# Optimization experiments

Hardware: AMD Instinct MI355X
Metric: run time of the kernel (lower is better)

The kernel has to match this reference:

```python
import jax, jax.numpy as jnp
import numpy as np

LOG2PI = float(np.log(2.0 * np.pi))
CLIP_LO, CLIP_HI = 1e-6, 1.0 - 1e-6


def gaussian_log_prob(X, mu):
    # X: (s, d), mu: (K, d) -> (s, K); unit-variance diagonal Normal.
    d = X.shape[-1]
    sq = (
        (X * X).sum(-1, keepdims=True)
        - 2.0 * (X @ mu.T)
        + (mu * mu).sum(-1)[None, :]
    )
    return -0.5 * (sq + d * LOG2PI)


def setup_inputs() -> dict:
    key = jax.random.key(0)
    kz, ks, kd, km1, km2 = jax.random.split(key, 5)
    s, K, n, dz = 60000, 200, 6, 64
    Z = jax.random.normal(kz, (s, dz), dtype=jnp.float32)
    S = jax.random.normal(ks, (s, 3), dtype=jnp.float32)
    D = jax.random.randint(kd, (s, n), 0, s, dtype=jnp.int64)
    sel_mu = jax.random.normal(km1, (K, dz), dtype=jnp.float32)
    spa_mu = jax.random.normal(km2, (K, 3), dtype=jnp.float32)
    return {"Z": Z, "S": S, "D": D, "sel_mu": sel_mu, "spa_mu": spa_mu}


def reference(Z, S, D, sel_mu, spa_mu):
    # point energy U: (s, K)
    U = -(gaussian_log_prob(Z, sel_mu) + gaussian_log_prob(S, spa_mu))
    Q = jax.nn.softmax(-U, axis=-1)  # temperature = 1.0
    # expected point energy: (s,)
    point = (Q * U).sum(-1)
    # doublet energy: gather neighbor rows, coassignment, potential, mask
    Qc = jnp.clip(Q, CLIP_LO, CLIP_HI)
    co = jnp.einsum('snk,sk->sn', Qc[D], Qc)  # (s, n)
    doublet = jnp.where(D < 0, 0.0, -jnp.log(co)).sum(-1)  # (s,)
    return point + doublet
```

## Files before the change

kernel.cpp:

```cpp
#include <hip/hip_runtime.h>
#include <math.h>

#define KK 200
#define NT 13
#define NNB 6

typedef __attribute__((ext_vector_type(8))) short short8;
typedef __attribute__((ext_vector_type(4))) float f32x4;
#define MFMA16 __builtin_amdgcn_mfma_f32_16x16x32_bf16

__device__ __forceinline__ unsigned short bfh(float f) {
    unsigned u = __float_as_uint(f);
    return (unsigned short)((u + 0x7fffu + ((u >> 16) & 1u)) >> 16);
}
__device__ __forceinline__ float bf2f(unsigned short h) {
    return __uint_as_float(((unsigned)h) << 16);
}
__device__ __forceinline__ short8 z8() {
    short8 v;
#pragma unroll
    for (int j = 0; j < 8; ++j) v[j] = 0;
    return v;
}
__device__ __forceinline__ void cv2(float f, short8& hi, short8& lo, int j) {
    unsigned short h = bfh(f);
    hi[j] = (short)h;
    lo[j] = (short)bfh(f - bf2f(h));
}

__global__ __launch_bounds__(512, 4) void
k_point(const float* __restrict__ Z, const float* __restrict__ S,
        const float* __restrict__ selmu, const float* __restrict__ spamu,
        unsigned short* __restrict__ Qc, float* __restrict__ pointbuf,
        int sRows, int mTiles)
{
    __shared__ short8 ldsBh[26 * 64];
    __shared__ short8 ldsBl[26 * 64];
    __shared__ uint2  ldsB2h[NT * 16];
    __shared__ uint2  ldsB2l[NT * 16];

    const int tid = threadIdx.x;

    for (int slot = tid; slot < 26 * 64; slot += 512) {
        int L = slot & 63, ts = slot >> 6;
        int t = ts >> 1, sstep = ts & 1;
        int n = t * 16 + (L & 15);
        int kb = sstep * 32 + (L >> 4) * 8;
        short8 hi = z8(), lo = z8();
        if (n < KK) {
            const float* mp = selmu + (size_t)n * 64 + kb;
            float4 a = *(const float4*)mp;
            float4 b = *(const float4*)(mp + 4);
            cv2(a.x, hi, lo, 0); cv2(a.y, hi, lo, 1); cv2(a.z, hi, lo, 2); cv2(a.w, hi, lo, 3);
            cv2(b.x, hi, lo, 4); cv2(b.y, hi, lo, 5); cv2(b.z, hi, lo, 6); cv2(b.w, hi, lo, 7);
        }
        ldsBh[slot] = hi;
        ldsBl[slot] = lo;
    }
    if (tid < NT * 16) {
        int n = tid;
        uint2 vh = make_uint2(0, 0), vl = make_uint2(0, 0);
        if (n < KK) {
            float p0 = spamu[n * 3 + 0], p1 = spamu[n * 3 + 1], p2 = spamu[n * 3 + 2];
            float nrm = p0 * p0 + p1 * p1 + p2 * p2;
            const float* mp = selmu + (size_t)n * 64;
#pragma unroll 8
            for (int k = 0; k < 64; ++k) { float m = mp[k]; nrm = fmaf(m, m, nrm); }
            nrm *= -0.5f;
            unsigned short h0 = bfh(p0), h1 = bfh(p1), h2 = bfh(p2), h3 = bfh(nrm);
            unsigned short g0 = bfh(p0 - bf2f(h0)), g1 = bfh(p1 - bf2f(h1));
            unsigned short g2 = bfh(p2 - bf2f(h2)), g3 = bfh(nrm - bf2f(h3));
            vh = make_uint2((unsigned)h0 | ((unsigned)h1 << 16), (unsigned)h2 | ((unsigned)h3 << 16));
            vl = make_uint2((unsigned)g0 | ((unsigned)g1 << 16), (unsigned)g2 | ((unsigned)g3 << 16));
        }
        ldsB2h[tid] = vh;
        ldsB2l[tid] = vl;
    }
    __syncthreads();

    const int lane = tid & 63;
    const int q = lane >> 4;
    const int li = lane & 15;

    const float cLog = 0.5f * 67.0f * 1.8378770664093453f;

    for (int wg = blockIdx.x * 8 + (tid >> 6); wg < mTiles; wg += gridDim.x * 8) {
        const int m0 = wg * 16;
        const int rowA = (m0 + li < sRows) ? (m0 + li) : (sRows - 1);

        const float* zr = Z + (size_t)rowA * 64 + q * 8;
        float4 z0 = *(const float4*)zr;
        float4 z1 = *(const float4*)(zr + 4);
        float4 z2 = *(const float4*)(zr + 32);
        float4 z3 = *(const float4*)(zr + 36);
        short8 ah0 = z8(), al0 = z8(), ah1 = z8(), al1 = z8();
        cv2(z0.x, ah0, al0, 0); cv2(z0.y, ah0, al0, 1); cv2(z0.z, ah0, al0, 2); cv2(z0.w, ah0, al0, 3);
        cv2(z1.x, ah0, al0, 4); cv2(z1.y, ah0, al0, 5); cv2(z1.z, ah0, al0, 6); cv2(z1.w, ah0, al0, 7);
        cv2(z2.x, ah1, al1, 0); cv2(z2.y, ah1, al1, 1); cv2(z2.z, ah1, al1, 2); cv2(z2.w, ah1, al1, 3);
        cv2(z3.x, ah1, al1, 4); cv2(z3.y, ah1, al1, 5); cv2(z3.z, ah1, al1, 6); cv2(z3.w, ah1, al1, 7);

        float zz = z0.x*z0.x + z0.y*z0.y + z0.z*z0.z + z0.w*z0.w
                 + z1.x*z1.x + z1.y*z1.y + z1.z*z1.z + z1.w*z1.w
                 + z2.x*z2.x + z2.y*z2.y + z2.z*z2.z + z2.w*z2.w
                 + z3.x*z3.x + z3.y*z3.y + z3.z*z3.z + z3.w*z3.w;
        zz += __shfl_xor(zz, 16);
        zz += __shfl_xor(zz, 32);

        float s0v = S[(size_t)rowA * 3 + 0];
        float s1v = S[(size_t)rowA * 3 + 1];
        float s2v = S[(size_t)rowA * 3 + 2];
        float cz = 0.5f * (zz + s0v * s0v + s1v * s1v + s2v * s2v) + cLog;

        short8 a2h = z8(), a2l = z8();
        if (lane < 16) {
            cv2(s0v, a2h, a2l, 0);
            cv2(s1v, a2h, a2l, 1);
            cv2(s2v, a2h, a2l, 2);
            a2h[3] = (short)bfh(1.0f);
        }

        f32x4 acc[NT];
#pragma unroll
        for (int t = 0; t < NT; ++t) { f32x4 zv = {0.f, 0.f, 0.f, 0.f}; acc[t] = zv; }

#pragma unroll
        for (int t = 0; t < NT; ++t) {
            short8 b0 = ldsBh[(t * 2 + 0) * 64 + lane];
            short8 b1 = ldsBh[(t * 2 + 1) * 64 + lane];
            short8 c0 = ldsBl[(t * 2 + 0) * 64 + lane];
            short8 c1 = ldsBl[(t * 2 + 1) * 64 + lane];
            uint2 bh2 = make_uint2(0, 0), bl2 = make_uint2(0, 0);
            if (lane < 16) { bh2 = ldsB2h[t * 16 + lane]; bl2 = ldsB2l[t * 16 + lane]; }
            short8 B2h = z8(), B2l = z8();
            B2h[0] = (short)(bh2.x & 0xffff); B2h[1] = (short)(bh2.x >> 16);
            B2h[2] = (short)(bh2.y & 0xffff); B2h[3] = (short)(bh2.y >> 16);
            B2l[0] = (short)(bl2.x & 0xffff); B2l[1] = (short)(bl2.x >> 16);
            B2l[2] = (short)(bl2.y & 0xffff); B2l[3] = (short)(bl2.y >> 16);

            acc[t] = MFMA16(ah0, b0, acc[t], 0, 0, 0);
            acc[t] = MFMA16(ah1, b1, acc[t], 0, 0, 0);
            acc[t] = MFMA16(al0, b0, acc[t], 0, 0, 0);
            acc[t] = MFMA16(al1, b1, acc[t], 0, 0, 0);
            acc[t] = MFMA16(ah0, c0, acc[t], 0, 0, 0);
            acc[t] = MFMA16(ah1, c1, acc[t], 0, 0, 0);
            acc[t] = MFMA16(a2h, B2h, acc[t], 0, 0, 0);
            acc[t] = MFMA16(a2l, B2h, acc[t], 0, 0, 0);
            acc[t] = MFMA16(a2h, B2l, acc[t], 0, 0, 0);
        }

#pragma unroll
        for (int r = 0; r < 4; ++r) {
            const int row = m0 + q * 4 + r;
            float e[NT];
            float mx = -1e30f;
#pragma unroll
            for (int t = 0; t < NT; ++t) {
                float v = acc[t][r];
                if (t == 12 && li >= 8) v = -1e30f;
                e[t] = v;
                mx = fmaxf(mx, v);
            }
            mx = fmaxf(mx, __shfl_xor(mx, 1));
            mx = fmaxf(mx, __shfl_xor(mx, 2));
            mx = fmaxf(mx, __shfl_xor(mx, 4));
            mx = fmaxf(mx, __shfl_xor(mx, 8));
            float sl = 0.f, pl = 0.f;
#pragma unroll
            for (int t = 0; t < NT; ++t) {
                float v = e[t];
                float ee = __expf(v - mx);
                sl += ee;
                pl = fmaf(ee, v, pl);
                e[t] = ee;
            }
#pragma unroll
            for (int off = 1; off <= 8; off <<= 1) {
                sl += __shfl_xor(sl, off);
                pl += __shfl_xor(pl, off);
            }
            float inv = 1.0f / sl;
            if (row < sRows) {
#pragma unroll
                for (int t = 0; t < NT; ++t) {
                    if (t < 12 || li < 8) {
                        float qv = fminf(fmaxf(e[t] * inv, 1e-6f), 1.0f - 1e-6f);
                        Qc[(size_t)row * KK + t * 16 + li] = bfh(qv);
                    }
                }
                float czr = __shfl(cz, q * 4 + r);
                if (li == 0) pointbuf[row] = czr - pl * inv;
            }
        }
    }
}

__global__ __launch_bounds__(256) void
k_doublet(const unsigned short* __restrict__ Qc, const float* __restrict__ pointbuf,
          const int* __restrict__ D, float* __restrict__ out, int sRows)
{
    const int lane = threadIdx.x & 63;
    const int wave = threadIdx.x >> 6;
    const int r0 = (blockIdx.x * 4 + wave) * 2;
    if (r0 >= sRows) return;
    const int half = lane >> 5;
    const int l = lane & 31;
    const int row = r0 + half;
    const bool rv = (row < sRows);
    const int rowc = rv ? row : r0;
    const bool act = (l < 25) && rv;
    const int lc = (l < 25) ? l : 0;

    uint4 ow = *(const uint4*)(Qc + (size_t)rowc * KK + lc * 8);
    float o0 = bf2f((unsigned short)(ow.x & 0xffff)), o1 = bf2f((unsigned short)(ow.x >> 16));
    float o2 = bf2f((unsigned short)(ow.y & 0xffff)), o3 = bf2f((unsigned short)(ow.y >> 16));
    float o4 = bf2f((unsigned short)(ow.z & 0xffff)), o5 = bf2f((unsigned short)(ow.z >> 16));
    float o6 = bf2f((unsigned short)(ow.w & 0xffff)), o7 = bf2f((unsigned short)(ow.w >> 16));

    int dj[NNB];
#pragma unroll
    for (int j = 0; j < NNB; ++j) dj[j] = D[(size_t)rowc * NNB + j];

    uint4 nbv[NNB];
#pragma unroll
    for (int j = 0; j < NNB; ++j) {
        int dd = (dj[j] >= 0) ? dj[j] : rowc;
        nbv[j] = *(const uint4*)(Qc + (size_t)dd * KK + lc * 8);
    }

    float pj[NNB];
#pragma unroll
    for (int j = 0; j < NNB; ++j) {
        uint4 nb = nbv[j];
        float t;
        t  = o0 * bf2f((unsigned short)(nb.x & 0xffff));
        t  = fmaf(o1, bf2f((unsigned short)(nb.x >> 16)), t);
        t  = fmaf(o2, bf2f((unsigned short)(nb.y & 0xffff)), t);
        t  = fmaf(o3, bf2f((unsigned short)(nb.y >> 16)), t);
        t  = fmaf(o4, bf2f((unsigned short)(nb.z & 0xffff)), t);
        t  = fmaf(o5, bf2f((unsigned short)(nb.z >> 16)), t);
        t  = fmaf(o6, bf2f((unsigned short)(nb.w & 0xffff)), t);
        t  = fmaf(o7, bf2f((unsigned short)(nb.w >> 16)), t);
        pj[j] = act ? t : 0.f;
    }
#pragma unroll
    for (int off = 1; off <= 16; off <<= 1) {
#pragma unroll
        for (int j = 0; j < NNB; ++j) pj[j] += __shfl_xor(pj[j], off);
    }
    float dbl = 0.f;
#pragma unroll
    for (int j = 0; j < NNB; ++j)
        if (dj[j] >= 0) dbl -= __logf(pj[j]);

    if (l == 0 && rv) out[row] = pointbuf[row] + dbl;
}

extern "C" void kernel_launch(void* const* d_in, const int* in_sizes, int n_in,
                              void* d_out, int out_size, void* d_ws, size_t ws_size,
                              hipStream_t stream) {
    const float* Z     = (const float*)d_in[0];
    const float* S     = (const float*)d_in[1];
    const int*   D     = (const int*)d_in[2];
    const float* selmu = (const float*)d_in[3];
    const float* spamu = (const float*)d_in[4];
    float* out = (float*)d_out;
    const int s = out_size;

    unsigned short* Qc = (unsigned short*)d_ws;
    float* pointbuf = (float*)((char*)d_ws + (size_t)s * KK * 2);

    const int mTiles = (s + 15) / 16;
    k_point<<<512, 512, 0, stream>>>(Z, S, selmu, spamu, Qc, pointbuf, s, mTiles);

    const int grid2 = ((s + 1) / 2 + 3) / 4;
    k_doublet<<<grid2, 256, 0, stream>>>(Qc, pointbuf, D, out, s);
}
```

Before: 111.7 us.

## Store scaled FP8 copy of Q for neighbor gathers and software-pipeline doublet rows

Result: no change. 111.3 us (-0.4%).

```diff
diff --git a/kernel.cpp b/kernel.cpp
--- a/kernel.cpp
+++ b/kernel.cpp
@@ -1,9 +1,11 @@
 #include <hip/hip_runtime.h>
+#include <hip/hip_fp16.h>
 #include <math.h>
 
 #define KK 200
 #define NT 13
 #define NNB 6
+#define Q8STRIDE 256
 
 typedef __attribute__((ext_vector_type(8))) short short8;
 typedef __attribute__((ext_vector_type(4))) float f32x4;
@@ -27,12 +29,22 @@
     hi[j] = (short)h;
     lo[j] = (short)bfh(f - bf2f(h));
 }
+__device__ __forceinline__ unsigned char f2e5(float f) {
+    unsigned short hb = __half_as_ushort(__float2half(f));
+    return (unsigned char)((hb + 0x7fu + ((hb >> 8) & 1u)) >> 8);
+}
+__device__ __forceinline__ void dec8(unsigned w, float* f) {
+    f[0] = __half2float(__ushort_as_half((unsigned short)((w << 8) & 0xff00u)));
+    f[1] = __half2float(__ushort_as_half((unsigned short)(w & 0xff00u)));
+    f[2] = __half2float(__ushort_as_half((unsigned short)((w >> 8) & 0xff00u)));
+    f[3] = __half2float(__ushort_as_half((unsigned short)((w >> 16) & 0xff00u)));
+}
 
 __global__ __launch_bounds__(512, 4) void
 k_point(const float* __restrict__ Z, const float* __restrict__ S,
         const float* __restrict__ selmu, const float* __restrict__ spamu,
-        unsigned short* __restrict__ Qc, float* __restrict__ pointbuf,
-        int sRows, int mTiles)
+        unsigned short* __restrict__ Qcb, unsigned char* __restrict__ Qc8,
+        float* __restrict__ pointbuf, int sRows, int mTiles)
 {
     __shared__ short8 ldsBh[26 * 64];
     __shared__ short8 ldsBl[26 * 64];
@@ -184,7 +196,8 @@
                 for (int t = 0; t < NT; ++t) {
                     if (t < 12 || li < 8) {
                         float qv = fminf(fmaxf(e[t] * inv, 1e-6f), 1.0f - 1e-6f);
-                        Qc[(size_t)row * KK + t * 16 + li] = bfh(qv);
+                        Qcb[(size_t)row * KK + t * 16 + li] = bfh(qv);
+                        Qc8[(size_t)row * Q8STRIDE + t * 16 + li] = f2e5(qv * 1024.0f);
                     }
                 }
                 float czr = __shfl(cz, q * 4 + r);
@@ -194,65 +207,90 @@
     }
 }
 
-__global__ __launch_bounds__(256) void
-k_doublet(const unsigned short* __restrict__ Qc, const float* __restrict__ pointbuf,
-          const int* __restrict__ D, float* __restrict__ out, int sRows)
+__global__ __launch_bounds__(512) void
+k_doublet(const unsigned short* __restrict__ Qcb, const unsigned char* __restrict__ Qc8,
+          const float* __restrict__ pointbuf, const int* __restrict__ D,
+          float* __restrict__ out, int sRows, int mTiles)
 {
+    const int wave = threadIdx.x >> 6;
     const int lane = threadIdx.x & 63;
-    const int wave = threadIdx.x >> 6;
-    const int r0 = (blockIdx.x * 4 + wave) * 2;
-    if (r0 >= sRows) return;
     const int half = lane >> 5;
     const int l = lane & 31;
-    const int row = r0 + half;
-    const bool rv = (row < sRows);
-    const int rowc = rv ? row : r0;
-    const bool act = (l < 25) && rv;
-    const int lc = (l < 25) ? l : 0;
-
-    uint4 ow = *(const uint4*)(Qc + (size_t)rowc * KK + lc * 8);
-    float o0 = bf2f((unsigned short)(ow.x & 0xffff)), o1 = bf2f((unsigned short)(ow.x >> 16));
-    float o2 = bf2f((unsigned short)(ow.y & 0xffff)), o3 = bf2f((unsigned short)(ow.y >> 16));
-    float o4 = bf2f((unsigned short)(ow.z & 0xffff)), o5 = bf2f((unsigned short)(ow.z >> 16));
-    float o6 = bf2f((unsigned short)(ow.w & 0xffff)), o7 = bf2f((unsigned short)(ow.w >> 16));
-
-    int dj[NNB];
+    const int sub = blockIdx.x >> 9;
+    const int b = blockIdx.x & 511;
+    const int T = b * 8 + wave;
+    if (T >= mTiles) return;
+    const int rbase = T * 16 + sub * 8;
+
+    const bool act = (l < 25);
+    const int lc = act ? l : 0;
+    const float LN1024 = 6.93147180559945f;
+
+    int   row  = rbase + half;
+    int   rowc = (row < sRows) ? row : (sRows - 1);
+    uint4 own  = *(const uint4*)(Qcb + (size_t)rowc * KK + lc * 8);
+    int   dj[NNB];
+    uint2 nb[NNB];
 #pragma unroll
     for (int j = 0; j < NNB; ++j) dj[j] = D[(size_t)rowc * NNB + j];
-
-    uint4 nbv[NNB];
 #pragma unroll
     for (int j = 0; j < NNB; ++j) {
         int dd = (dj[j] >= 0) ? dj[j] : rowc;
-        nbv[j] = *(const uint4*)(Qc + (size_t)dd * KK + lc * 8);
-    }
-
-    float pj[NNB];
-#pragma unroll
-    for (int j = 0; j < NNB; ++j) {
-        uint4 nb = nbv[j];
-        float t;
-        t  = o0 * bf2f((unsigned short)(nb.x & 0xffff));
-        t  = fmaf(o1, bf2f((unsigned short)(nb.x >> 16)), t);
-        t  = fmaf(o2, bf2f((unsigned short)(nb.y & 0xffff)), t);
-        t  = fmaf(o3, bf2f((unsigned short)(nb.y >> 16)), t);
-        t  = fmaf(o4, bf2f((unsigned short)(nb.z & 0xffff)), t);
-        t  = fmaf(o5, bf2f((unsigned short)(nb.z >> 16)), t);
-        t  = fmaf(o6, bf2f((unsigned short)(nb.w & 0xffff)), t);
-        t  = fmaf(o7, bf2f((unsigned short)(nb.w >> 16)), t);
-        pj[j] = act ? t : 0.f;
-    }
-#pragma unroll
-    for (int off = 1; off <= 16; off <<= 1) {
-#pragma unroll
-        for (int j = 0; j < NNB; ++j) pj[j] += __shfl_xor(pj[j], off);
-    }
-    float dbl = 0.f;
-#pragma unroll
-    for (int j = 0; j < NNB; ++j)
-        if (dj[j] >= 0) dbl -= __logf(pj[j]);
-
-    if (l == 0 && rv) out[row] = pointbuf[row] + dbl;
+        nb[j] = *(const uint2*)(Qc8 + (size_t)dd * Q8STRIDE + lc * 8);
+    }
+
+    for (int it = 0; it < 4; ++it) {
+        int   rowN = 0, rowcN = 0;
+        uint4 ownN = make_uint4(0, 0, 0, 0);
+        int   djN[NNB];
+        uint2 nbN[NNB];
+        if (it < 3) {
+            rowN  = rbase + (it + 1) * 2 + half;
+            rowcN = (rowN < sRows) ? rowN : (sRows - 1);
+            ownN  = *(const uint4*)(Qcb + (size_t)rowcN * KK + lc * 8);
+#pragma unroll
+            for (int j = 0; j < NNB; ++j) djN[j] = D[(size_t)rowcN * NNB + j];
+#pragma unroll
+            for (int j = 0; j < NNB; ++j) {
+                int dd = (djN[j] >= 0) ? djN[j] : rowcN;
+                nbN[j] = *(const uint2*)(Qc8 + (size_t)dd * Q8STRIDE + lc * 8);
+            }
+        }
+
+        float o[8];
+        o[0] = bf2f((unsigned short)(own.x & 0xffff)); o[1] = bf2f((unsigned short)(own.x >> 16));
+        o[2] = bf2f((unsigned short)(own.y & 0xffff)); o[3] = bf2f((unsigned short)(own.y >> 16));
+        o[4] = bf2f((unsigned short)(own.z & 0xffff)); o[5] = bf2f((unsigned short)(own.z >> 16));
+        o[6] = bf2f((unsigned short)(own.w & 0xffff)); o[7] = bf2f((unsigned short)(own.w >> 16));
+
+        float pj[NNB];
+#pragma unroll
+        for (int j = 0; j < NNB; ++j) {
+            float bv[8];
+            dec8(nb[j].x, bv);
+            dec8(nb[j].y, bv + 4);
+            float t = o[0] * bv[0];
+            t = fmaf(o[1], bv[1], t); t = fmaf(o[2], bv[2], t); t = fmaf(o[3], bv[3], t);
+            t = fmaf(o[4], bv[4], t); t = fmaf(o[5], bv[5], t); t = fmaf(o[6], bv[6], t);
+            t = fmaf(o[7], bv[7], t);
+            pj[j] = act ? t : 0.f;
+        }
+#pragma unroll
+        for (int off = 1; off <= 16; off <<= 1) {
+#pragma unroll
+            for (int j = 0; j < NNB; ++j) pj[j] += __shfl_xor(pj[j], off);
+        }
+        float dbl = 0.f;
+#pragma unroll
+        for (int j = 0; j < NNB; ++j)
+            if (dj[j] >= 0) dbl += LN1024 - __logf(pj[j]);
+
+        if (l == 0 && row < sRows) out[row] = pointbuf[row] + dbl;
+
+        row = rowN; rowc = rowcN; own = ownN;
+#pragma unroll
+        for (int j = 0; j < NNB; ++j) { dj[j] = djN[j]; nb[j] = nbN[j]; }
+    }
 }
 
 extern "C" void kernel_launch(void* const* d_in, const int* in_sizes, int n_in,
@@ -266,12 +304,15 @@
     float* out = (float*)d_out;
     const int s = out_size;
 
-    unsigned short* Qc = (unsigned short*)d_ws;
-    float* pointbuf = (float*)((char*)d_ws + (size_t)s * KK * 2);
+    const size_t qcbB = (size_t)s * KK * 2;
+    const size_t qc8B = (size_t)s * Q8STRIDE;
+    unsigned short* Qcb = (unsigned short*)d_ws;
+    unsigned char*  Qc8 = (unsigned char*)d_ws + qcbB;
+    float* pointbuf = (float*)((char*)d_ws + qcbB + qc8B);
 
     const int mTiles = (s + 15) / 16;
-    k_point<<<512, 512, 0, stream>>>(Z, S, selmu, spamu, Qc, pointbuf, s, mTiles);
-
-    const int grid2 = ((s + 1) / 2 + 3) / 4;
-    k_doublet<<<grid2, 256, 0, stream>>>(Qc, pointbuf, D, out, s);
-}
+    const int grid1 = (mTiles + 7) / 8;
+    k_point<<<grid1, 512, 0, stream>>>(Z, S, selmu, spamu, Qcb, Qc8, pointbuf, s, mTiles);
+
+    k_doublet<<<1024, 512, 0, stream>>>(Qcb, Qc8, pointbuf, D, out, s, mTiles);
+}
```
